# Performance work log

Hardware: AMD Instinct MI355X
Metric: run time of the kernel (lower is better)

Reference implementation:

```python
import jax, jax.numpy as jnp
import numpy as np

T = 17            # tensor side -> 289 flat channels
C = T * T
EPS = 1e-5


def tconv(x, W1, W2, b, stride):
    """Tucker-2 tensor conv: per offset (i,j) OUT = W1[i,j] @ X @ W2[i,j].
    x: [B, a*bt, H, W]; W1: [kh,kw,T,a]; W2: [kh,kw,bt,T]; b: [289].
    Equivalent dense kernel K[(p,q),(a,b),i,j] = W1[i,j,p,a]*W2[i,j,b,q]."""
    kh, kw, _, a = W1.shape
    bt = W2.shape[2]
    K = jnp.einsum('ijpa,ijbq->pqabij', W1, W2).reshape(C, a * bt, kh, kw)
    pad = (kh - 1) // 2
    y = jax.lax.conv_general_dilated(
        x, K, (stride, stride), [(pad, pad), (pad, pad)],
        dimension_numbers=('NCHW', 'OIHW', 'NCHW'))
    return y + b.reshape(1, C, 1, 1)


def bn(x, g, bta):
    # training-mode BN over flattened 17x17 tensor channels (biased var)
    m = jnp.mean(x, axis=(0, 2, 3), keepdims=True)
    v = jnp.var(x, axis=(0, 2, 3), keepdims=True)
    return g.reshape(1, -1, 1, 1) * (x - m) * jax.lax.rsqrt(v + EPS) + bta.reshape(1, -1, 1, 1)


def prelu(x, a):
    return jnp.where(x >= 0, x, a * x)


def setup_inputs() -> dict:
    key = jax.random.key(0)
    ks = jax.random.split(key, 8)
    x = jax.random.normal(ks[0], (32, 3, 160, 160), dtype=jnp.float32)
    s = 0.1
    feat_W1 = jax.random.normal(ks[1], (3, 3, T, 3), dtype=jnp.float32) * s
    feat_W2 = jax.random.normal(ks[2], (3, 3, 1, T), dtype=jnp.float32) * s
    feat_b = jnp.zeros((C,), dtype=jnp.float32)
    # 27 1x1 convs: shortcuts 0..8, block k uses 9+2k and 10+2k
    c11_W1 = jax.random.normal(ks[3], (27, 1, 1, T, T), dtype=jnp.float32) * s
    c11_W2 = jax.random.normal(ks[4], (27, 1, 1, T, T), dtype=jnp.float32) * s
    c11_b = jnp.zeros((27, C), dtype=jnp.float32)
    # 9 3x3 convs (one per block)
    c33_W1 = jax.random.normal(ks[5], (9, 3, 3, T, T), dtype=jnp.float32) * s
    c33_W2 = jax.random.normal(ks[6], (9, 3, 3, T, T), dtype=jnp.float32) * s
    c33_b = jnp.zeros((9, C), dtype=jnp.float32)
    # 37 BNs: 0=features, 1+j shortcut j, 10+3k..12+3k block k
    bn_g = jnp.ones((37, C), dtype=jnp.float32)
    bn_bt = jnp.zeros((37, C), dtype=jnp.float32)
    # 19 PReLUs: 0=features, block k uses 1+2k, 2+2k
    prelu_a = jnp.full((19,), 0.25, dtype=jnp.float32)
    return {"x": x, "feat_W1": feat_W1, "feat_W2": feat_W2, "feat_b": feat_b,
            "c11_W1": c11_W1, "c11_W2": c11_W2, "c11_b": c11_b,
            "c33_W1": c33_W1, "c33_W2": c33_W2, "c33_b": c33_b,
            "bn_g": bn_g, "bn_bt": bn_bt, "prelu_a": prelu_a}


def reference(x, feat_W1, feat_W2, feat_b, c11_W1, c11_W2, c11_b,
              c33_W1, c33_W2, c33_b, bn_g, bn_bt, prelu_a):
    # features: 3x3 s2 tensor conv [3,1]->[17,17], BN, PReLU
    h = tconv(x, feat_W1, feat_W2, feat_b, 2)
    h = prelu(bn(h, bn_g[0], bn_bt[0]), prelu_a[0])
    # 9 residual blocks; blocks 0,1 downsample by 2
    for k in range(9):
        s = 2 if k < 2 else 1
        i1, i2 = 9 + 2 * k, 10 + 2 * k
        j = 10 + 3 * k
        idn = bn(tconv(h, c11_W1[k], c11_W2[k], c11_b[k], s), bn_g[1 + k], bn_bt[1 + k])
        y = prelu(bn(tconv(h, c11_W1[i1], c11_W2[i1], c11_b[i1], 1), bn_g[j], bn_bt[j]), prelu_a[1 + 2 * k])
        y = prelu(bn(tconv(y, c33_W1[k], c33_W2[k], c33_b[k], s), bn_g[j + 1], bn_bt[j + 1]), prelu_a[2 + 2 * k])
        y = bn(tconv(y, c11_W1[i2], c11_W2[i2], c11_b[i2], 1), bn_g[j + 2], bn_bt[j + 2])
        h = y + idn
    return h  # [B, 289, 20, 20] == torch [B,1,20,20,17,17] flattened
```

## Files before the change

### kernel.cpp

```cpp
#include <hip/hip_runtime.h>
#include <hip/hip_bf16.h>

#define EPS 1e-5f
#define CSTR 292
#define PST 580
#define FPIX 15

typedef __hip_bfloat16 bf16;
typedef short s16x8 __attribute__((ext_vector_type(8)));
typedef float f32x4 __attribute__((ext_vector_type(4)));
typedef unsigned short u16x4 __attribute__((ext_vector_type(4)));
typedef unsigned short u16x8 __attribute__((ext_vector_type(8)));

__device__ inline float bf2f(unsigned short u) {
    union { unsigned int i; float f; } z; z.i = ((unsigned int)u) << 16; return z.f;
}
__device__ inline unsigned short f2bf(float f) {
    union { bf16 h; unsigned short u; } z; z.h = __float2bfloat16(f); return z.u;
}
__device__ inline unsigned short f2bf_trunc(float f) {
    union { float f; unsigned int u; } z; z.f = f; return (unsigned short)(z.u >> 16);
}

__device__ __forceinline__ void prep_frag(const float* w1, const float* w2,
                                          bf16* o, int kt, int nt, int l) {
#pragma unroll
    for (int e = 0; e < 8; ++e) {
        int k = kt * 32 + ((l >> 4) << 3) + e;
        int n = nt * 16 + (l & 15);
        float v = 0.f;
        if (k < 289 && n < 289)
            v = w1[(n / 17) * 17 + (k / 17)] * w2[(k % 17) * 17 + (n % 17)];
        o[e] = __float2bfloat16(v);
    }
}

__global__ void prep11_all_k(const float* __restrict__ W1all, const float* __restrict__ W2all,
                             bf16* __restrict__ Bsw) {
    int bi = blockIdx.x;
    int cv = bi / 190, r = bi - cv * 190;
    int kt = r / 19, nt = r - kt * 19;
    prep_frag(W1all + (size_t)cv * 289, W2all + (size_t)cv * 289,
              Bsw + (size_t)bi * 512 + threadIdx.x * 8, kt, nt, threadIdx.x);
}

__global__ void prep33_k(const float* __restrict__ W1, const float* __restrict__ W2,
                         bf16* __restrict__ Bsw) {
    int bi = blockIdx.x;
    int tap = bi / 190; int r = bi - tap * 190;
    int kt = r / 19, nt = r - kt * 19;
    prep_frag(W1 + (size_t)tap * 289, W2 + (size_t)tap * 289,
              Bsw + (size_t)bi * 512 + threadIdx.x * 8, kt, nt, threadIdx.x);
}

__global__ void prep33all_k(const float* __restrict__ W1, const float* __restrict__ W2,
                            bf16* __restrict__ Bsw) {
    int fi = blockIdx.x * 4 + (threadIdx.x >> 6);
    int l = threadIdx.x & 63;
    int kb = fi / 1710, r = fi - kb * 1710;
    int tap = r / 190; int rr = r - tap * 190;
    int kt = rr / 19, nt = rr - kt * 19;
    const float* w1 = W1 + (long)(kb + 1) * 9 * 289 + (long)tap * 289;
    const float* w2 = W2 + (long)(kb + 1) * 9 * 289 + (long)tap * 289;
    prep_frag(w1, w2, Bsw + (size_t)fi * 512 + l * 8, kt, nt, l);
}

__global__ __launch_bounds__(256) void feat_k(
    const float* __restrict__ x, bf16* __restrict__ out,
    const float* __restrict__ W1, const float* __restrict__ W2,
    float* __restrict__ partial) {
    __shared__ float W1s[459], W2s[153];
    __shared__ float S[289], SS[289];
    __shared__ bf16 T[FPIX][292];
    int tid = threadIdx.x;
    for (int i = tid; i < 459; i += 256) W1s[i] = W1[i];
    for (int i = tid; i < 153; i += 256) W2s[i] = W2[i];
    for (int i = tid; i < 289; i += 256) { S[i] = 0.f; SS[i] = 0.f; }
    if (tid < FPIX * 3) T[tid / 3][289 + tid % 3] = __float2bfloat16(0.f);
    int lp = tid / 17, p = tid - lp * 17;
    bool act = tid < 255;
    float sacc[17], qacc[17];
#pragma unroll
    for (int q = 0; q < 17; ++q) { sacc[q] = 0.f; qacc[q] = 0.f; }
    const int NT = (204800 + FPIX - 1) / FPIX;
    __syncthreads();
    for (int t = blockIdx.x; t < NT; t += gridDim.x) {
        int pix0 = t * FPIX;
        int pix = pix0 + lp;
        if (act && pix < 204800) {
            int b = pix / 6400; int rr = pix - b * 6400;
            int oh = rr / 80, ow = rr - oh * 80;
            float y[17];
#pragma unroll
            for (int q = 0; q < 17; ++q) y[q] = 0.f;
            for (int di = 0; di < 3; ++di) {
                int ih = oh * 2 + di - 1;
                if (ih < 0 || ih >= 160) continue;
                for (int dj = 0; dj < 3; ++dj) {
                    int iw = ow * 2 + dj - 1;
                    if (iw < 0 || iw >= 160) continue;
                    int k = di * 3 + dj;
                    long xb = (long)b * 76800 + ih * 160 + iw;
                    float dot = W1s[(k * 17 + p) * 3 + 0] * x[xb]
                              + W1s[(k * 17 + p) * 3 + 1] * x[xb + 25600]
                              + W1s[(k * 17 + p) * 3 + 2] * x[xb + 51200];
#pragma unroll
                    for (int q = 0; q < 17; ++q) y[q] += dot * W2s[k * 17 + q];
                }
            }
#pragma unroll
            for (int q = 0; q < 17; ++q) {
                bf16 h = __float2bfloat16(y[q]);
                T[lp][p * 17 + q] = h;
                float vv = __bfloat162float(h);
                sacc[q] += vv; qacc[q] += vv * vv;
            }
        }
        __syncthreads();
        int nv = 204800 - pix0; if (nv > FPIX) nv = FPIX;
        for (int idx = tid; idx < nv * 73; idx += 256) {
            int row = idx / 73, j = idx - row * 73;
            *(u16x4*)(out + (long)(pix0 + row) * CSTR + j * 4) =
                *(const u16x4*)(&T[row][j * 4]);
        }
        __syncthreads();
    }
    if (act) {
#pragma unroll
        for (int q = 0; q < 17; ++q) {
            atomicAdd(&S[p * 17 + q], sacc[q]);
            atomicAdd(&SS[p * 17 + q], qacc[q]);
        }
    }
    __syncthreads();
    for (int i = tid; i < 289; i += 256) {
        partial[(long)blockIdx.x * PST + i] = S[i];
        partial[(long)blockIdx.x * PST + 290 + i] = SS[i];
    }
}

template <typename TI, typename TO, int TAPS, bool DUAL, int MT>
__global__ __launch_bounds__(256, MT == 2 ? 3 : 5) void gemm_k(
    const TI* __restrict__ in1, const TI* __restrict__ in2, TO* __restrict__ out,
    const bf16* __restrict__ Bs, const float* __restrict__ scshAll, int bn1, int bn2,
    const float* __restrict__ alphaPtr, float* __restrict__ partial,
    int Hin, int Win, int Hout, int Wout, int stride) {
    constexpr int MROWS = 16 * MT;
    constexpr int SITS = (37 * MROWS + 255) / 256;
    static_assert(MROWS * 304 * sizeof(TO) <= 2 * MROWS * 640, "epilogue must fit As");
    __shared__ char As[2 * MROWS * 640];
    __shared__ float sc1[296], sh1[296];
    __shared__ float sc2[DUAL ? 296 : 1], sh2[DUAL ? 296 : 1];
    __shared__ long gb00[MROWS];
    __shared__ int ihw0[MROWS];
    int tid = threadIdx.x;
    int HWin = Hin * Win, HWout = Hout * Wout;
    int pix0 = blockIdx.x * MROWS;
    for (int i = tid; i < 296; i += 256) {
        int cc = i < 289 ? i : 0;
        sc1[i] = scshAll[bn1 * 578 + cc]; sh1[i] = scshAll[bn1 * 578 + 289 + cc];
        if constexpr (DUAL) {
            sc2[i] = scshAll[bn2 * 578 + cc]; sh2[i] = scshAll[bn2 * 578 + 289 + cc];
        }
    }
    if (tid < MROWS) {
        int op = pix0 + tid;
        int b = op / HWout; int rr = op - b * HWout;
        int oh = rr / Wout, ow = rr - oh * Wout;
        int ih0 = oh * stride + (TAPS == 9 ? -1 : 0);
        int iw0 = ow * stride + (TAPS == 9 ? -1 : 0);
        gb00[tid] = ((long)b * HWin + (long)ih0 * Win + iw0) * CSTR;
        ihw0[tid] = ((ih0 + 1) << 16) | (iw0 + 1);
    }
    if (tid < 8 * MROWS) {
        int half = tid / (4 * MROWS), r = (tid >> 2) & (MROWS - 1), c = tid & 3;
        int byte = (r * 640 + 576 + c * 16) ^ ((r & 7) << 4);
        *(u16x8*)(As + half * (MROWS * 640) + byte) = (u16x8){0, 0, 0, 0, 0, 0, 0, 0};
    }
    float alpha = DUAL ? 0.f : *alphaPtr;
    int w = tid >> 6, l = tid & 63;
    int nt0 = w * 5;
    int lane_n = l & 15;
    int kbyte = (l >> 4) << 4;
    f32x4 acc[MT][5];
#pragma unroll
    for (int m = 0; m < MT; ++m)
#pragma unroll
        for (int j = 0; j < 5; ++j) acc[m][j] = (f32x4){0.f, 0.f, 0.f, 0.f};
    __syncthreads();

    bool cact[SITS]; int cih[SITS], ciw[SITS], cwb[SITS], ck0[SITS]; long cgb[SITS];
#pragma unroll
    for (int it = 0; it < SITS; ++it) {
        int cid = it * 256 + tid;
        cact[it] = cid < 37 * MROWS;
        int row = cact[it] ? cid / 37 : 0;
        int j = cid - row * 37;
        ck0[it] = j * 8;
        cgb[it] = gb00[row] + j * 8;
        int pk = ihw0[row];
        cih[it] = (pk >> 16) - 1; ciw[it] = (pk & 0xffff) - 1;
        cwb[it] = (row * 640 + j * 16) ^ ((row & 7) << 4);
    }
    bool vld[SITS];
    u16x4 rh1[SITS][2]; f32x4 rf1[SITS][2];
    u16x4 rh2[DUAL ? SITS : 1][2]; f32x4 rf2[DUAL ? SITS : 1][2];

    auto LOAD = [&](int tap) {
        int di = (TAPS == 9) ? tap / 3 : 0;
        int dj = (TAPS == 9) ? tap - di * 3 : 0;
        long toff = (long)(di * Win + dj) * CSTR;
#pragma unroll
        for (int it = 0; it < SITS; ++it) {
            vld[it] = false;
            if (cact[it]) {
                int ih = cih[it] + di, iw = ciw[it] + dj;
                if (ih >= 0 && ih < Hin && iw >= 0 && iw < Win) {
                    vld[it] = true;
                    long gb = cgb[it] + toff;
                    if constexpr (sizeof(TI) == 2) {
                        rh1[it][0] = *(const u16x4*)((const bf16*)in1 + gb);
                        rh1[it][1] = *(const u16x4*)((const bf16*)in1 + gb + 4);
                        if constexpr (DUAL) {
                            rh2[it][0] = *(const u16x4*)((const bf16*)in2 + gb);
                            rh2[it][1] = *(const u16x4*)((const bf16*)in2 + gb + 4);
                        }
                    } else {
                        rf1[it][0] = *(const f32x4*)((const float*)in1 + gb);
                        rf1[it][1] = *(const f32x4*)((const float*)in1 + gb + 4);
                        if constexpr (DUAL) {
                            rf2[it][0] = *(const f32x4*)((const float*)in2 + gb);
                            rf2[it][1] = *(const f32x4*)((const float*)in2 + gb + 4);
                        }
                    }
                }
            }
        }
    };

    auto WRITE = [&]() {
#pragma unroll
        for (int it = 0; it < SITS; ++it) {
            if (!cact[it]) continue;
            float v[8];
            if (vld[it]) {
                int k0 = ck0[it];
                float r[8];
                if constexpr (sizeof(TI) == 2) {
#pragma unroll
                    for (int e = 0; e < 4; ++e) {
                        r[e] = bf2f(rh1[it][0][e]); r[4 + e] = bf2f(rh1[it][1][e]);
                    }
                } else {
#pragma unroll
                    for (int e = 0; e < 4; ++e) {
                        r[e] = rf1[it][0][e]; r[4 + e] = rf1[it][1][e];
                    }
                }
#pragma unroll
                for (int e = 0; e < 8; ++e) v[e] = sc1[k0 + e] * r[e] + sh1[k0 + e];
                if constexpr (DUAL) {
                    float q[8];
                    if constexpr (sizeof(TI) == 2) {
#pragma unroll
                        for (int e = 0; e < 4; ++e) {
                            q[e] = bf2f(rh2[it][0][e]); q[4 + e] = bf2f(rh2[it][1][e]);
                        }
                    } else {
#pragma unroll
                        for (int e = 0; e < 4; ++e) {
                            q[e] = rf2[it][0][e]; q[4 + e] = rf2[it][1][e];
                        }
                    }
#pragma unroll
                    for (int e = 0; e < 8; ++e) v[e] += sc2[k0 + e] * q[e] + sh2[k0 + e];
                } else {
#pragma unroll
                    for (int e = 0; e < 8; ++e) v[e] = v[e] >= 0.f ? v[e] : alpha * v[e];
                }
#pragma unroll
                for (int e = 0; e < 8; ++e) if (ck0[it] + e > 288) v[e] = 0.f;
            } else {
#pragma unroll
                for (int e = 0; e < 8; ++e) v[e] = 0.f;
            }
            u16x4 hi0, hi1, lo0, lo1;
#pragma unroll
            for (int e = 0; e < 4; ++e) {
                unsigned short h = f2bf(v[e]);
                hi0[e] = h; lo0[e] = f2bf_trunc(v[e] - bf2f(h));
                unsigned short h2 = f2bf(v[4 + e]);
                hi1[e] = h2; lo1[e] = f2bf_trunc(v[4 + e] - bf2f(h2));
            }
            int byte = cwb[it];
            *(u16x4*)(As + byte) = hi0;
            *(u16x4*)(As + byte + 8) = hi1;
            *(u16x4*)(As + MROWS * 640 + byte) = lo0;
            *(u16x4*)(As + MROWS * 640 + byte + 8) = lo1;
        }
    };

    LOAD(0);
#pragma unroll 1
    for (int tap = 0; tap < TAPS; ++tap) {
        WRITE();
        if (tap + 1 < TAPS) LOAD(tap + 1);
        __syncthreads();
        const bf16* bp = Bs + (size_t)tap * 97280 + (size_t)l * 8;
        int swz = (lane_n & 7) << 4;
        __builtin_amdgcn_s_setprio(1);
#pragma unroll 2
        for (int kt = 0; kt < 10; ++kt) {
            s16x8 ah[MT], al[MT];
#pragma unroll
            for (int m = 0; m < MT; ++m) {
                int ro = ((m * 16 + lane_n) * 640 + kbyte + kt * 64) ^ swz;
                ah[m] = *(const s16x8*)(As + ro);
                al[m] = *(const s16x8*)(As + MROWS * 640 + ro);
            }
#pragma unroll
            for (int j = 0; j < 5; ++j) {
                if (j < 4 || w < 3) {
                    s16x8 bfr = *(const s16x8*)(bp + (size_t)(kt * 19 + nt0 + j) * 512);
#pragma unroll
                    for (int m = 0; m < MT; ++m) {
                        acc[m][j] = __builtin_amdgcn_mfma_f32_16x16x32_bf16(
                            ah[m], bfr, acc[m][j], 0, 0, 0);
                        acc[m][j] = __builtin_amdgcn_mfma_f32_16x16x32_bf16(
                            al[m], bfr, acc[m][j], 0, 0, 0);
                    }
                }
            }
        }
        __builtin_amdgcn_s_setprio(0);
        __syncthreads();
    }
    {
#pragma unroll
        for (int j = 0; j < 5; ++j) {
            float s = 0.f, ss = 0.f;
            if (j < 4 || w < 3) {
#pragma unroll
                for (int m = 0; m < MT; ++m)
#pragma unroll
                    for (int e = 0; e < 4; ++e) {
                        float v = acc[m][j][e];
                        s += v; ss += v * v;
                    }
            }
            s += __shfl_xor(s, 16); ss += __shfl_xor(ss, 16);
            s += __shfl_xor(s, 32); ss += __shfl_xor(ss, 32);
            int n = (nt0 + j) * 16 + lane_n;
            if (l < 16 && n < 289 && (j < 4 || w < 3)) {
                partial[(long)blockIdx.x * PST + n] = s;
                partial[(long)blockIdx.x * PST + 290 + n] = ss;
            }
        }
    }
    {
        TO* ep = (TO*)As;
        int re = (l >> 4) << 2;
#pragma unroll
        for (int m = 0; m < MT; ++m) {
#pragma unroll
            for (int j = 0; j < 5; ++j) {
                if (j < 4 || w < 3) {
                    int n = (nt0 + j) * 16 + lane_n;
#pragma unroll
                    for (int e = 0; e < 4; ++e) {
                        if constexpr (sizeof(TO) == 2)
                            ep[(m * 16 + re + e) * 304 + n] = __float2bfloat16(acc[m][j][e]);
                        else
                            ((float*)ep)[(m * 16 + re + e) * 304 + n] = acc[m][j][e];
                    }
                }
            }
        }
        __syncthreads();
        for (int cid = tid; cid < MROWS * 73; cid += 256) {
            int row = cid / 73, j = cid - row * 73;
            long g = (long)(pix0 + row) * CSTR + j * 4;
            if constexpr (sizeof(TO) == 2) {
                u16x4 v = *(const u16x4*)((const bf16*)ep + row * 304 + j * 4);
                *(u16x4*)((bf16*)out + g) = v;
            } else {
                f32x4 v = *(const f32x4*)((const float*)ep + row * 304 + j * 4);
                *(f32x4*)((float*)out + g) = v;
            }
        }
    }
}

__global__ __launch_bounds__(256, 3) void gemm2_k(
    const float* __restrict__ in1, const float* __restrict__ in2,
    float* __restrict__ out1, float* __restrict__ out2,
    const bf16* __restrict__ Bs1, const bf16* __restrict__ Bs2,
    const float* __restrict__ scshAll, int bn1, int bn2,
    float* __restrict__ partial1, float* __restrict__ partial2) {
    constexpr int MROWS = 16;
    __shared__ char As[2 * MROWS * 640];
    __shared__ float sc1[296], sh1[296], sc2[296], sh2[296];
    int tid = threadIdx.x;
    for (int i = tid; i < 296; i += 256) {
        int cc = i < 289 ? i : 0;
        sc1[i] = scshAll[bn1 * 578 + cc]; sh1[i] = scshAll[bn1 * 578 + 289 + cc];
        sc2[i] = scshAll[bn2 * 578 + cc]; sh2[i] = scshAll[bn2 * 578 + 289 + cc];
    }
    if (tid < 128) {
        int half = tid >> 6, r = (tid >> 2) & 15, c = tid & 3;
        int byte = (r * 640 + 576 + c * 16) ^ ((r & 7) << 4);
        *(u16x8*)(As + half * (MROWS * 640) + byte) = (u16x8){0, 0, 0, 0, 0, 0, 0, 0};
    }
    int pix0 = blockIdx.x * MROWS;
    int w = tid >> 6, l = tid & 63;
    int nt0 = w * 5, lane_n = l & 15, kbyte = (l >> 4) << 4;
    f32x4 acc1[5], acc2[5];
#pragma unroll
    for (int j = 0; j < 5; ++j) {
        acc1[j] = (f32x4){0.f, 0.f, 0.f, 0.f};
        acc2[j] = (f32x4){0.f, 0.f, 0.f, 0.f};
    }
    __syncthreads();
#pragma unroll
    for (int it = 0; it < 3; ++it) {
        int cid = it * 256 + tid;
        if (cid < 592) {
            int row = cid / 37, j = cid - row * 37, k0 = j * 8;
            long gb = (long)(pix0 + row) * CSTR + k0;
            f32x4 a = *(const f32x4*)(in1 + gb), b = *(const f32x4*)(in1 + gb + 4);
            f32x4 c = *(const f32x4*)(in2 + gb), d = *(const f32x4*)(in2 + gb + 4);
            float v[8];
#pragma unroll
            for (int e = 0; e < 4; ++e) {
                v[e] = sc1[k0 + e] * a[e] + sh1[k0 + e] + sc2[k0 + e] * c[e] + sh2[k0 + e];
                v[4 + e] = sc1[k0 + 4 + e] * b[e] + sh1[k0 + 4 + e]
                         + sc2[k0 + 4 + e] * d[e] + sh2[k0 + 4 + e];
            }
#pragma unroll
            for (int e = 0; e < 8; ++e) if (k0 + e > 288) v[e] = 0.f;
            u16x4 hi0, hi1, lo0, lo1;
#pragma unroll
            for (int e = 0; e < 4; ++e) {
                unsigned short h = f2bf(v[e]);
                hi0[e] = h; lo0[e] = f2bf_trunc(v[e] - bf2f(h));
                unsigned short h2 = f2bf(v[4 + e]);
                hi1[e] = h2; lo1[e] = f2bf_trunc(v[4 + e] - bf2f(h2));
            }
            int byte = (row * 640 + j * 16) ^ ((row & 7) << 4);
            *(u16x4*)(As + byte) = hi0;
            *(u16x4*)(As + byte + 8) = hi1;
            *(u16x4*)(As + MROWS * 640 + byte) = lo0;
            *(u16x4*)(As + MROWS * 640 + byte + 8) = lo1;
        }
    }
    __syncthreads();
    const bf16* bp1 = Bs1 + (size_t)l * 8;
    const bf16* bp2 = Bs2 + (size_t)l * 8;
    int swz = (lane_n & 7) << 4;
    __builtin_amdgcn_s_setprio(1);
#pragma unroll 2
    for (int kt = 0; kt < 10; ++kt) {
        int ro = (lane_n * 640 + kbyte + kt * 64) ^ swz;
        s16x8 ah = *(const s16x8*)(As + ro);
        s16x8 al = *(const s16x8*)(As + MROWS * 640 + ro);
#pragma unroll
        for (int j = 0; j < 5; ++j) {
            if (j < 4 || w < 3) {
                size_t fo = (size_t)(kt * 19 + nt0 + j) * 512;
                s16x8 b1 = *(const s16x8*)(bp1 + fo);
                acc1[j] = __builtin_amdgcn_mfma_f32_16x16x32_bf16(ah, b1, acc1[j], 0, 0, 0);
                acc1[j] = __builtin_amdgcn_mfma_f32_16x16x32_bf16(al, b1, acc1[j], 0, 0, 0);
                s16x8 b2 = *(const s16x8*)(bp2 + fo);
                acc2[j] = __builtin_amdgcn_mfma_f32_16x16x32_bf16(ah, b2, acc2[j], 0, 0, 0);
                acc2[j] = __builtin_amdgcn_mfma_f32_16x16x32_bf16(al, b2, acc2[j], 0, 0, 0);
            }
        }
    }
    __builtin_amdgcn_s_setprio(0);
    __syncthreads();
#pragma unroll
    for (int j = 0; j < 5; ++j) {
        float s1 = 0.f, q1 = 0.f, s2 = 0.f, q2 = 0.f;
        if (j < 4 || w < 3) {
#pragma unroll
            for (int e = 0; e < 4; ++e) {
                float v1 = acc1[j][e]; s1 += v1; q1 += v1 * v1;
                float v2 = acc2[j][e]; s2 += v2; q2 += v2 * v2;
            }
        }
        s1 += __shfl_xor(s1, 16); q1 += __shfl_xor(q1, 16);
        s1 += __shfl_xor(s1, 32); q1 += __shfl_xor(q1, 32);
        s2 += __shfl_xor(s2, 16); q2 += __shfl_xor(q2, 16);
        s2 += __shfl_xor(s2, 32); q2 += __shfl_xor(q2, 32);
        int n = (nt0 + j) * 16 + lane_n;
        if (l < 16 && n < 289 && (j < 4 || w < 3)) {
            partial1[(long)blockIdx.x * PST + n] = s1;
            partial1[(long)blockIdx.x * PST + 290 + n] = q1;
            partial2[(long)blockIdx.x * PST + n] = s2;
            partial2[(long)blockIdx.x * PST + 290 + n] = q2;
        }
    }
    float* ep = (float*)As;
    int re = (l >> 4) << 2;
#pragma unroll
    for (int pass = 0; pass < 2; ++pass) {
        const f32x4* ac = pass ? acc2 : acc1;
        float* op = pass ? out2 : out1;
#pragma unroll
        for (int j = 0; j < 5; ++j) {
            if (j < 4 || w < 3) {
                int n = (nt0 + j) * 16 + lane_n;
#pragma unroll
                for (int e = 0; e < 4; ++e) ep[(re + e) * 304 + n] = ac[j][e];
            }
        }
        __syncthreads();
        for (int cid = tid; cid < MROWS * 73; cid += 256) {
            int row = cid / 73, j = cid - row * 73;
            long g = (long)(pix0 + row) * CSTR + j * 4;
            f32x4 v = *(const f32x4*)(ep + row * 304 + j * 4);
            *(f32x4*)(op + g) = v;
        }
        __syncthreads();
    }
}

__device__ __forceinline__ void fin_one(const float* partial, const float* g,
                                        const float* bt, float* scshAll,
                                        int bnid, float invN, int GN, int c) {
    float s = 0.f, ss = 0.f;
    for (int k = threadIdx.x; k < GN; k += 256) {
        s += partial[(long)k * PST + c];
        ss += partial[(long)k * PST + 290 + c];
    }
    for (int o = 32; o; o >>= 1) { s += __shfl_down(s, o); ss += __shfl_down(ss, o); }
    __shared__ float ls[4], lss[4];
    int w = threadIdx.x >> 6;
    if ((threadIdx.x & 63) == 0) { ls[w] = s; lss[w] = ss; }
    __syncthreads();
    if (threadIdx.x == 0) {
        s = ls[0] + ls[1] + ls[2] + ls[3];
        ss = lss[0] + lss[1] + lss[2] + lss[3];
        float m = s * invN;
        float v = ss * invN - m * m;
        float sc = g[c] * rsqrtf(v + EPS);
        scshAll[bnid * 578 + c] = sc;
        scshAll[bnid * 578 + 289 + c] = bt[c] - m * sc;
    }
}

__global__ void finalize_k(const float* __restrict__ partial, const float* __restrict__ g,
                           const float* __restrict__ bt, float* __restrict__ scshAll,
                           int bnid, float invN, int GN) {
    fin_one(partial, g, bt, scshAll, bnid, invN, GN, blockIdx.x);
}

__global__ void finalize2v_k(const float* __restrict__ pA, const float* __restrict__ pB,
                             const float* __restrict__ gAll, const float* __restrict__ btAll,
                             float* __restrict__ scshAll, int bnA, int bnB,
                             float invA, int GNa, float invB, int GNb) {
    int q = blockIdx.x / 289, c = blockIdx.x - q * 289;
    const float* p = q ? pB : pA;
    int bnid = q ? bnB : bnA;
    fin_one(p, gAll + bnid * 289, btAll + bnid * 289, scshAll, bnid,
            q ? invB : invA, q ? GNb : GNa, c);
}

__global__ void final_k(const float* __restrict__ y3, const float* __restrict__ idn,
                        float* __restrict__ out, const float* __restrict__ scshAll,
                        int bnY, int bnI) {
    __shared__ float T[32][305];
    int bi = blockIdx.x;
    int b = bi / 13, t0 = (bi - (bi / 13) * 13) * 32;
    int tid = threadIdx.x;
    int nhw = 400 - t0; if (nhw > 32) nhw = 32;
    for (int idx = tid; idx < 32 * 304; idx += 256) {
        int hwl = idx / 304, c = idx - hwl * 304;
        float v = 0.f;
        if (hwl < nhw && c < 289) {
            long pix = (long)b * 400 + t0 + hwl;
            v = scshAll[bnY * 578 + c] * y3[pix * CSTR + c] + scshAll[bnY * 578 + 289 + c]
              + scshAll[bnI * 578 + c] * idn[pix * CSTR + c] + scshAll[bnI * 578 + 289 + c];
        }
        T[hwl][c] = v;
    }
    __syncthreads();
    for (int idx = tid; idx < 289 * 32; idx += 256) {
        int c = idx >> 5, hwl = idx & 31;
        if (hwl < nhw)
            out[((long)b * 289 + c) * 400 + t0 + hwl] = T[hwl][c];
    }
}

extern "C" void kernel_launch(void* const* d_in, const int* in_sizes, int n_in,
                              void* d_out, int out_size, void* d_ws, size_t ws_size,
                              hipStream_t stream) {
    const float* x     = (const float*)d_in[0];
    const float* fW1   = (const float*)d_in[1];
    const float* fW2   = (const float*)d_in[2];
    const float* c11W1 = (const float*)d_in[4];
    const float* c11W2 = (const float*)d_in[5];
    const float* c33W1 = (const float*)d_in[7];
    const float* c33W2 = (const float*)d_in[8];
    const float* bng   = (const float*)d_in[10];
    const float* bnbt  = (const float*)d_in[11];
    const float* pa    = (const float*)d_in[12];
    float* outp = (float*)d_out;

    char* base = (char*)d_ws;
    bf16*  A    = (bf16*)base;
    bf16*  Bb   = (bf16*)(base + 119603200L);
    bf16*  Cb   = (bf16*)(base + 149504000L);
    float* scsh = (float*)(base + 179404800L);
    bf16*  B33s = (bf16*)(base + 179490368L);
    size_t need = 181241408L;
    if (ws_size < need) return;
    float* D = (float*)base;
    float* E = (float*)(base + 14950400L);
    float* F = (float*)(base + 29900800L);
    float* partialA = (float*)(base + 50000000L);
    bf16*  B33all   = (bf16*)(base + 100000000L);

    float* partial = (float*)d_out;
    bf16*  B11all  = (bf16*)((char*)d_out + 7424000L);
    float* partial2 = partial + 800L * PST;
    float* partialBig = (float*)Cb;

    const float inv80 = 1.f / 204800.f, inv40 = 1.f / 51200.f, inv20 = 1.f / 12800.f;

#define B11(cv) (B11all + (size_t)(cv) * 97280)
#define B33A(cv) (B33all + (size_t)((cv) - 1) * 875520)
#define FIN(P, bnid, invN, GN) finalize_k<<<dim3(289), dim3(256), 0, stream>>>( \
        (P), bng + (bnid) * 289, bnbt + (bnid) * 289, scsh, (bnid), (invN), (GN))

    prep11_all_k<<<dim3(27 * 190), dim3(64), 0, stream>>>(c11W1, c11W2, B11all);

    feat_k<<<dim3(2048), dim3(256), 0, stream>>>(x, A, fW1, fW2, partial);
    FIN(partial, 0, inv80, 2048);

    gemm_k<bf16, bf16, 1, false, 2><<<dim3(1600), dim3(256), 0, stream>>>(
        A, nullptr, Bb, B11(0), scsh, 0, 0, pa + 0, partial, 80, 80, 40, 40, 2);
    gemm_k<bf16, bf16, 1, false, 2><<<dim3(6400), dim3(256), 0, stream>>>(
        A, nullptr, A, B11(9), scsh, 0, 0, pa + 0, partialBig, 80, 80, 80, 80, 1);
    finalize2v_k<<<dim3(578), dim3(256), 0, stream>>>(
        partial, partialBig, bng, bnbt, scsh, 1, 10, inv40, 1600, inv80, 6400);
    prep33_k<<<dim3(1710), dim3(64), 0, stream>>>(c33W1, c33W2, B33s);
    gemm_k<bf16, bf16, 9, false, 2><<<dim3(1600), dim3(256), 0, stream>>>(
        A, nullptr, Cb, B33s, scsh, 10, 0, pa + 1, partial, 80, 80, 40, 40, 2);
    prep33all_k<<<dim3(3420), dim3(256), 0, stream>>>(c33W1, c33W2, B33all);
    FIN(partial, 11, inv40, 1600);
    gemm_k<bf16, bf16, 1, false, 2><<<dim3(1600), dim3(256), 0, stream>>>(
        Cb, nullptr, Cb, B11(10), scsh, 11, 0, pa + 2, partial, 40, 40, 40, 40, 1);
    FIN(partial, 12, inv40, 1600);

    gemm_k<bf16, float, 1, true, 1><<<dim3(800), dim3(256), 0, stream>>>(
        Cb, Bb, D, B11(1), scsh, 12, 1, nullptr, partialA, 40, 40, 20, 20, 2);
    gemm_k<bf16, bf16, 1, true, 2><<<dim3(1600), dim3(256), 0, stream>>>(
        Cb, Bb, Cb, B11(11), scsh, 12, 1, nullptr, partial, 40, 40, 40, 40, 1);
    finalize2v_k<<<dim3(578), dim3(256), 0, stream>>>(
        partialA, partial, bng, bnbt, scsh, 2, 13, inv20, 800, inv40, 1600);
    gemm_k<bf16, float, 9, false, 2><<<dim3(400), dim3(256), 0, stream>>>(
        Cb, nullptr, E, B33A(1), scsh, 13, 0, pa + 3, partial, 40, 40, 20, 20, 2);
    FIN(partial, 14, inv20, 400);
    gemm_k<float, float, 1, false, 1><<<dim3(800), dim3(256), 0, stream>>>(
        E, nullptr, E, B11(12), scsh, 14, 0, pa + 4, partial, 20, 20, 20, 20, 1);
    FIN(partial, 15, inv20, 800);

    float *X = E, *Y = D, *Z = F;
    for (int k = 2; k < 9; ++k) {
        gemm2_k<<<dim3(800), dim3(256), 0, stream>>>(
            X, Y, Z, X, B11(k), B11(9 + 2 * k), scsh, 9 + 3 * k, k, partial, partial2);
        finalize2v_k<<<dim3(578), dim3(256), 0, stream>>>(
            partial, partial2, bng, bnbt, scsh, 1 + k, 10 + 3 * k,
            inv20, 800, inv20, 800);
        gemm_k<float, float, 9, false, 2><<<dim3(400), dim3(256), 0, stream>>>(
            X, nullptr, Y, B33A(k), scsh, 10 + 3 * k, 0, pa + 1 + 2 * k, partial,
            20, 20, 20, 20, 1);
        FIN(partial, 11 + 3 * k, inv20, 400);
        gemm_k<float, float, 1, false, 1><<<dim3(800), dim3(256), 0, stream>>>(
            Y, nullptr, Y, B11(10 + 2 * k), scsh, 11 + 3 * k, 0, pa + 2 + 2 * k, partial,
            20, 20, 20, 20, 1);
        FIN(partial, 12 + 3 * k, inv20, 800);
        float* t = X; X = Y; Y = Z; Z = t;
    }
    final_k<<<dim3(416), dim3(256), 0, stream>>>(X, Y, outp, scsh, 36, 9);
}
```

Baseline: 1.891 ms.

## Fuse BN statistic finalization into GEMM kernels via atomic accumulators

For the 20x20 stages, GEMM epilogues now atomically add per-channel sums and sums of squares into small global accumulators instead of writing per-block partials. The consuming kernel derives BN scale and shift itself in its prologue. This removes the separate finalize kernel launches, about 23 of them, and their serialization gaps. The cost is global atomic contention across 400-800 blocks, recomputing the coefficients in every block, an extra memset, and floating-point ordering that is no longer deterministic.

```diff
diff --git a/kernel.cpp b/kernel.cpp
--- a/kernel.cpp
+++ b/kernel.cpp
@@ -20,6 +20,20 @@
 }
 __device__ inline unsigned short f2bf_trunc(float f) {
     union { float f; unsigned int u; } z; z.f = f; return (unsigned short)(z.u >> 16);
+}
+
+__device__ inline void bn_coef(const float* scshAll, const float* gAll,
+                               const float* btAll, const float* iAcc,
+                               int bn, float invN, int c, float& sc, float& sh) {
+    if (iAcc) {
+        float m = iAcc[c] * invN;
+        float v = iAcc[290 + c] * invN - m * m;
+        sc = gAll[bn * 289 + c] * rsqrtf(v + EPS);
+        sh = btAll[bn * 289 + c] - m * sc;
+    } else {
+        sc = scshAll[bn * 578 + c];
+        sh = scshAll[bn * 578 + 289 + c];
+    }
 }
 
 __device__ __forceinline__ void prep_frag(const float* w1, const float* w2,
@@ -144,6 +158,9 @@
     const TI* __restrict__ in1, const TI* __restrict__ in2, TO* __restrict__ out,
     const bf16* __restrict__ Bs, const float* __restrict__ scshAll, int bn1, int bn2,
     const float* __restrict__ alphaPtr, float* __restrict__ partial,
+    const float* __restrict__ gAll, const float* __restrict__ btAll,
+    const float* __restrict__ iAcc1, const float* __restrict__ iAcc2, float invNin,
+    float* __restrict__ oAcc,
     int Hin, int Win, int Hout, int Wout, int stride) {
     constexpr int MROWS = 16 * MT;
     constexpr int SITS = (37 * MROWS + 255) / 256;
@@ -158,9 +175,12 @@
     int pix0 = blockIdx.x * MROWS;
     for (int i = tid; i < 296; i += 256) {
         int cc = i < 289 ? i : 0;
-        sc1[i] = scshAll[bn1 * 578 + cc]; sh1[i] = scshAll[bn1 * 578 + 289 + cc];
+        float sc, sh;
+        bn_coef(scshAll, gAll, btAll, iAcc1, bn1, invNin, cc, sc, sh);
+        sc1[i] = sc; sh1[i] = sh;
         if constexpr (DUAL) {
-            sc2[i] = scshAll[bn2 * 578 + cc]; sh2[i] = scshAll[bn2 * 578 + 289 + cc];
+            bn_coef(scshAll, gAll, btAll, iAcc2, bn2, invNin, cc, sc, sh);
+            sc2[i] = sc; sh2[i] = sh;
         }
     }
     if (tid < MROWS) {
@@ -352,8 +372,13 @@
             s += __shfl_xor(s, 32); ss += __shfl_xor(ss, 32);
             int n = (nt0 + j) * 16 + lane_n;
             if (l < 16 && n < 289 && (j < 4 || w < 3)) {
-                partial[(long)blockIdx.x * PST + n] = s;
-                partial[(long)blockIdx.x * PST + 290 + n] = ss;
+                if (oAcc) {
+                    atomicAdd(&oAcc[n], s);
+                    atomicAdd(&oAcc[290 + n], ss);
+                } else {
+                    partial[(long)blockIdx.x * PST + n] = s;
+                    partial[(long)blockIdx.x * PST + 290 + n] = ss;
+                }
             }
         }
     }
@@ -396,15 +421,20 @@
     float* __restrict__ out1, float* __restrict__ out2,
     const bf16* __restrict__ Bs1, const bf16* __restrict__ Bs2,
     const float* __restrict__ scshAll, int bn1, int bn2,
-    float* __restrict__ partial1, float* __restrict__ partial2) {
+    const float* __restrict__ gAll, const float* __restrict__ btAll,
+    const float* __restrict__ iAcc1, const float* __restrict__ iAcc2, float invNin,
+    float* __restrict__ oAcc1, float* __restrict__ oAcc2) {
     constexpr int MROWS = 16;
     __shared__ char As[2 * MROWS * 640];
     __shared__ float sc1[296], sh1[296], sc2[296], sh2[296];
     int tid = threadIdx.x;
     for (int i = tid; i < 296; i += 256) {
         int cc = i < 289 ? i : 0;
-        sc1[i] = scshAll[bn1 * 578 + cc]; sh1[i] = scshAll[bn1 * 578 + 289 + cc];
-        sc2[i] = scshAll[bn2 * 578 + cc]; sh2[i] = scshAll[bn2 * 578 + 289 + cc];
+        float sc, sh;
+        bn_coef(scshAll, gAll, btAll, iAcc1, bn1, invNin, cc, sc, sh);
+        sc1[i] = sc; sh1[i] = sh;
+        bn_coef(scshAll, gAll, btAll, iAcc2, bn2, invNin, cc, sc, sh);
+        sc2[i] = sc; sh2[i] = sh;
     }
     if (tid < 128) {
         int half = tid >> 6, r = (tid >> 2) & 15, c = tid & 3;
@@ -494,10 +524,8 @@
         s2 += __shfl_xor(s2, 32); q2 += __shfl_xor(q2, 32);
         int n = (nt0 + j) * 16 + lane_n;
         if (l < 16 && n < 289 && (j < 4 || w < 3)) {
-            partial1[(long)blockIdx.x * PST + n] = s1;
-            partial1[(long)blockIdx.x * PST + 290 + n] = q1;
-            partial2[(long)blockIdx.x * PST + n] = s2;
-            partial2[(long)blockIdx.x * PST + 290 + n] = q2;
+            atomicAdd(&oAcc1[n], s1); atomicAdd(&oAcc1[290 + n], q1);
+            atomicAdd(&oAcc2[n], s2); atomicAdd(&oAcc2[290 + n], q2);
         }
     }
     float* ep = (float*)As;
@@ -567,20 +595,31 @@
 }
 
 __global__ void final_k(const float* __restrict__ y3, const float* __restrict__ idn,
-                        float* __restrict__ out, const float* __restrict__ scshAll,
-                        int bnY, int bnI) {
+                        float* __restrict__ out,
+                        const float* __restrict__ gAll, const float* __restrict__ btAll,
+                        const float* __restrict__ iAccY, const float* __restrict__ iAccI,
+                        int bnY, int bnI, float invN) {
     __shared__ float T[32][305];
+    __shared__ float scY[289], shY[289], scI[289], shI[289];
+    int tid = threadIdx.x;
+    for (int i = tid; i < 289; i += 256) {
+        float sc, sh;
+        bn_coef(nullptr, gAll, btAll, iAccY, bnY, invN, i, sc, sh);
+        scY[i] = sc; shY[i] = sh;
+        bn_coef(nullptr, gAll, btAll, iAccI, bnI, invN, i, sc, sh);
+        scI[i] = sc; shI[i] = sh;
+    }
+    __syncthreads();
     int bi = blockIdx.x;
     int b = bi / 13, t0 = (bi - (bi / 13) * 13) * 32;
-    int tid = threadIdx.x;
     int nhw = 400 - t0; if (nhw > 32) nhw = 32;
     for (int idx = tid; idx < 32 * 304; idx += 256) {
         int hwl = idx / 304, c = idx - hwl * 304;
         float v = 0.f;
         if (hwl < nhw && c < 289) {
             long pix = (long)b * 400 + t0 + hwl;
-            v = scshAll[bnY * 578 + c] * y3[pix * CSTR + c] + scshAll[bnY * 578 + 289 + c]
-              + scshAll[bnI * 578 + c] * idn[pix * CSTR + c] + scshAll[bnI * 578 + 289 + c];
+            v = scY[c] * y3[pix * CSTR + c] + shY[c]
+              + scI[c] * idn[pix * CSTR + c] + shI[c];
         }
         T[hwl][c] = v;
     }
@@ -619,17 +658,20 @@
     float* E = (float*)(base + 14950400L);
     float* F = (float*)(base + 29900800L);
     float* partialA = (float*)(base + 50000000L);
+    float* accT     = (float*)(base + 60000000L);
     bf16*  B33all   = (bf16*)(base + 100000000L);
 
     float* partial = (float*)d_out;
     bf16*  B11all  = (bf16*)((char*)d_out + 7424000L);
-    float* partial2 = partial + 800L * PST;
     float* partialBig = (float*)Cb;
 
     const float inv80 = 1.f / 204800.f, inv40 = 1.f / 51200.f, inv20 = 1.f / 12800.f;
 
 #define B11(cv) (B11all + (size_t)(cv) * 97280)
 #define B33A(cv) (B33all + (size_t)((cv) - 1) * 875520)
+#define ACC(s) (accT + (s) * 580)
+#define ACCK(ki, j) (accT + (2 + (ki) * 4 + (j)) * 580)
+#define NOACC bng, bnbt, nullptr, nullptr, 0.f, nullptr
 #define FIN(P, bnid, invN, GN) finalize_k<<<dim3(289), dim3(256), 0, stream>>>( \
         (P), bng + (bnid) * 289, bnbt + (bnid) * 289, scsh, (bnid), (invN), (GN))
 
@@ -639,49 +681,56 @@
     FIN(partial, 0, inv80, 2048);
 
     gemm_k<bf16, bf16, 1, false, 2><<<dim3(1600), dim3(256), 0, stream>>>(
-        A, nullptr, Bb, B11(0), scsh, 0, 0, pa + 0, partial, 80, 80, 40, 40, 2);
+        A, nullptr, Bb, B11(0), scsh, 0, 0, pa + 0, partial, NOACC,
+        80, 80, 40, 40, 2);
     gemm_k<bf16, bf16, 1, false, 2><<<dim3(6400), dim3(256), 0, stream>>>(
-        A, nullptr, A, B11(9), scsh, 0, 0, pa + 0, partialBig, 80, 80, 80, 80, 1);
+        A, nullptr, A, B11(9), scsh, 0, 0, pa + 0, partialBig, NOACC,
+        80, 80, 80, 80, 1);
     finalize2v_k<<<dim3(578), dim3(256), 0, stream>>>(
         partial, partialBig, bng, bnbt, scsh, 1, 10, inv40, 1600, inv80, 6400);
     prep33_k<<<dim3(1710), dim3(64), 0, stream>>>(c33W1, c33W2, B33s);
     gemm_k<bf16, bf16, 9, false, 2><<<dim3(1600), dim3(256), 0, stream>>>(
-        A, nullptr, Cb, B33s, scsh, 10, 0, pa + 1, partial, 80, 80, 40, 40, 2);
+        A, nullptr, Cb, B33s, scsh, 10, 0, pa + 1, partial, NOACC,
+        80, 80, 40, 40, 2);
     prep33all_k<<<dim3(3420), dim3(256), 0, stream>>>(c33W1, c33W2, B33all);
+    hipMemsetAsync(accT, 0, 30 * 580 * sizeof(float), stream);
     FIN(partial, 11, inv40, 1600);
     gemm_k<bf16, bf16, 1, false, 2><<<dim3(1600), dim3(256), 0, stream>>>(
-        Cb, nullptr, Cb, B11(10), scsh, 11, 0, pa + 2, partial, 40, 40, 40, 40, 1);
+        Cb, nullptr, Cb, B11(10), scsh, 11, 0, pa + 2, partial, NOACC,
+        40, 40, 40, 40, 1);
     FIN(partial, 12, inv40, 1600);
 
     gemm_k<bf16, float, 1, true, 1><<<dim3(800), dim3(256), 0, stream>>>(
-        Cb, Bb, D, B11(1), scsh, 12, 1, nullptr, partialA, 40, 40, 20, 20, 2);
+        Cb, Bb, D, B11(1), scsh, 12, 1, nullptr, partialA, NOACC,
+        40, 40, 20, 20, 2);
     gemm_k<bf16, bf16, 1, true, 2><<<dim3(1600), dim3(256), 0, stream>>>(
-        Cb, Bb, Cb, B11(11), scsh, 12, 1, nullptr, partial, 40, 40, 40, 40, 1);
+        Cb, Bb, Cb, B11(11), scsh, 12, 1, nullptr, partial, NOACC,
+        40, 40, 40, 40, 1);
     finalize2v_k<<<dim3(578), dim3(256), 0, stream>>>(
         partialA, partial, bng, bnbt, scsh, 2, 13, inv20, 800, inv40, 1600);
     gemm_k<bf16, float, 9, false, 2><<<dim3(400), dim3(256), 0, stream>>>(
-        Cb, nullptr, E, B33A(1), scsh, 13, 0, pa + 3, partial, 40, 40, 20, 20, 2);
-    FIN(partial, 14, inv20, 400);
+        Cb, nullptr, E, B33A(1), scsh, 13, 0, pa + 3, partial,
+        bng, bnbt, nullptr, nullptr, 0.f, ACC(0), 40, 40, 20, 20, 2);
     gemm_k<float, float, 1, false, 1><<<dim3(800), dim3(256), 0, stream>>>(
-        E, nullptr, E, B11(12), scsh, 14, 0, pa + 4, partial, 20, 20, 20, 20, 1);
-    FIN(partial, 15, inv20, 800);
+        E, nullptr, E, B11(12), scsh, 14, 0, pa + 4, partial,
+        bng, bnbt, ACC(0), nullptr, inv20, ACC(1), 20, 20, 20, 20, 1);
 
     float *X = E, *Y = D, *Z = F;
     for (int k = 2; k < 9; ++k) {
+        int ki = k - 2;
+        const float* iA1 = (k == 2) ? ACC(1) : ACCK(ki - 1, 3);
+        const float* iA2 = (k == 2) ? nullptr : ACCK(ki - 1, 0);
         gemm2_k<<<dim3(800), dim3(256), 0, stream>>>(
-            X, Y, Z, X, B11(k), B11(9 + 2 * k), scsh, 9 + 3 * k, k, partial, partial2);
-        finalize2v_k<<<dim3(578), dim3(256), 0, stream>>>(
-            partial, partial2, bng, bnbt, scsh, 1 + k, 10 + 3 * k,
-            inv20, 800, inv20, 800);
+            X, Y, Z, X, B11(k), B11(9 + 2 * k), scsh, 9 + 3 * k, k,
+            bng, bnbt, iA1, iA2, inv20, ACCK(ki, 0), ACCK(ki, 1));
         gemm_k<float, float, 9, false, 2><<<dim3(400), dim3(256), 0, stream>>>(
             X, nullptr, Y, B33A(k), scsh, 10 + 3 * k, 0, pa + 1 + 2 * k, partial,
-            20, 20, 20, 20, 1);
-        FIN(partial, 11 + 3 * k, inv20, 400);
+            bng, bnbt, ACCK(ki, 1), nullptr, inv20, ACCK(ki, 2), 20, 20, 20, 20, 1);
         gemm_k<float, float, 1, false, 1><<<dim3(800), dim3(256), 0, stream>>>(
             Y, nullptr, Y, B11(10 + 2 * k), scsh, 11 + 3 * k, 0, pa + 2 + 2 * k, partial,
-            20, 20, 20, 20, 1);
-        FIN(partial, 12 + 3 * k, inv20, 800);
+            bng, bnbt, ACCK(ki, 2), nullptr, inv20, ACCK(ki, 3), 20, 20, 20, 20, 1);
         float* t = X; X = Y; Y = Z; Z = t;
     }
-    final_k<<<dim3(416), dim3(256), 0, stream>>>(X, Y, outp, scsh, 36, 9);
-}
+    final_k<<<dim3(416), dim3(256), 0, stream>>>(
+        X, Y, outp, bng, bnbt, ACCK(6, 3), ACCK(6, 0), 36, 9, inv20);
+}
```

After: 2.517 ms. 33.1% more time.
